# Performance work log

Measured on AMD Instinct MI355X. Metric: run time of the kernel, lower is better.

Reference implementation:

```python
import jax, jax.numpy as jnp
import numpy as np

THRESHOLD = 0.5
NEG_POS_RATIO = 3
ALPHA = 1.0
B, P, C, O = 64, 8732, 81, 32


def setup_inputs() -> dict:
    key = jax.random.key(0)
    k1, k2, k3, k4, k5, k6 = jax.random.split(key, 6)
    pred_locs = jax.random.normal(k1, (B, P, 4), dtype=jnp.float32)
    pred_scores = jax.random.normal(k2, (B, P, C), dtype=jnp.float32)
    # valid ground-truth corner boxes: sample center/size, convert to xy, clip to [0,1]
    ctr = jax.random.uniform(k3, (B, O, 2), minval=0.1, maxval=0.9)
    wh = jax.random.uniform(k4, (B, O, 2), minval=0.05, maxval=0.4)
    boxes = jnp.clip(jnp.concatenate([ctr - wh / 2, ctr + wh / 2], axis=-1), 0.0, 1.0)
    labels = jax.random.randint(k5, (B, O), 1, C, dtype=jnp.int64)
    pc = jax.random.uniform(k6, (P, 2), minval=0.05, maxval=0.95)
    pwh = jax.random.uniform(jax.random.fold_in(k6, 1), (P, 2), minval=0.05, maxval=0.3)
    priors_cxcy = jnp.concatenate([pc, pwh], axis=-1)
    return {"pred_locs": pred_locs, "pred_scores": pred_scores,
            "boxes": boxes, "labels": labels, "priors_cxcy": priors_cxcy}


def _jaccard(b, priors_xy):
    # b: [O,4] xy, priors_xy: [P,4] xy -> [O,P]
    lo = jnp.maximum(b[:, None, :2], priors_xy[None, :, :2])
    hi = jnp.minimum(b[:, None, 2:], priors_xy[None, :, 2:])
    inter = jnp.prod(jnp.clip(hi - lo, 0.0), axis=-1)
    area_b = jnp.prod(b[:, 2:] - b[:, :2], axis=-1)
    area_p = jnp.prod(priors_xy[:, 2:] - priors_xy[:, :2], axis=-1)
    return inter / (area_b[:, None] + area_p[None, :] - inter)


def _forward(pred_locs, pred_scores, boxes, labels, priors_cxcy):
    priors_xy = jnp.concatenate([priors_cxcy[:, :2] - priors_cxcy[:, 2:] / 2,
                                 priors_cxcy[:, :2] + priors_cxcy[:, 2:] / 2], axis=1)
    n_obj = boxes.shape[1]

    def match(b, l):
        ov = _jaccard(b, priors_xy)                      # [O,P]
        ov_fp = jnp.max(ov, axis=0)                      # [P]
        obj_fp = jnp.argmax(ov, axis=0)                  # [P]
        prior_fo = jnp.argmax(ov, axis=1)                # [O]
        obj_fp = obj_fp.at[prior_fo].set(jnp.arange(n_obj))
        ov_fp = ov_fp.at[prior_fo].set(1.0)
        lab = jnp.where(ov_fp < THRESHOLD, 0, l[obj_fp]) # [P]
        pt = b[obj_fp]                                   # [P,4] xy
        c = jnp.concatenate([(pt[:, 2:] + pt[:, :2]) / 2, pt[:, 2:] - pt[:, :2]], axis=1)
        g = jnp.concatenate([(c[:, :2] - priors_cxcy[:, :2]) / (priors_cxcy[:, 2:] / 10),
                             jnp.log(c[:, 2:] / priors_cxcy[:, 2:]) * 5], axis=1)
        return g, lab

    true_locs, true_classes = jax.vmap(match)(boxes, labels)  # [B,P,4], [B,P]

    pos = true_classes != 0                                   # [B,P]
    n_pos = jnp.sum(pos, axis=1)                              # [B]
    n_pos_total = jnp.sum(n_pos).astype(pred_locs.dtype)

    # L1Loss (mean over positive elements, 4 coords each)
    loc_abs = jnp.abs(pred_locs - true_locs) * pos[..., None].astype(pred_locs.dtype)
    loc_loss = jnp.sum(loc_abs) / (n_pos_total * 4.0)

    # per-prior cross entropy
    logp = jax.nn.log_softmax(pred_scores, axis=-1)           # [B,P,C]
    ce = -jnp.take_along_axis(logp, true_classes[..., None], axis=-1)[..., 0]  # [B,P]

    posf = pos.astype(ce.dtype)
    conf_pos_sum = jnp.sum(ce * posf)
    conf_neg = jnp.where(pos, 0.0, ce)
    conf_neg_sorted = -jnp.sort(-conf_neg, axis=1)            # descending
    ranks = jnp.arange(ce.shape[1])[None, :]
    hard = ranks < (NEG_POS_RATIO * n_pos)[:, None]
    conf_hard_neg_sum = jnp.sum(conf_neg_sorted * hard.astype(ce.dtype))

    conf_loss = (conf_hard_neg_sum + conf_pos_sum) / n_pos_total
    return conf_loss + ALPHA * loc_loss


def reference(pred_locs, pred_scores, boxes, labels, priors_cxcy):
    return _forward(pred_locs, pred_scores, boxes, labels, priors_cxcy)
```

## Files before the change

kernel.cpp:

```cpp
#include <hip/hip_runtime.h>

#define BB 64
#define PP 8732
#define OO 32
#define CC 81
#define NEGPOS 3
#define NCH_B 32
#define CHB 273
#define NCEB 137

typedef float f32x4 __attribute__((ext_vector_type(4), aligned(4)));

#define WS_BESTP  0
#define WS_CENEG  (WS_BESTP + BB*NCH_B*OO*8)
#define WS_CEPOS  (WS_CENEG + BB*PP*4)
#define WS_LSUMB  (WS_CEPOS + BB*NCEB*16)
#define WS_NPOSB  (WS_LSUMB + BB*NCEB*16)
#define WS_HARDB  (WS_NPOSB + BB*NCEB*16)
#define WS_DONE   (WS_HARDB + BB*4)

__global__ __launch_bounds__(512) void match_obj(
    const float* __restrict__ boxes, const float* __restrict__ priors,
    unsigned long long* __restrict__ bestp, int* __restrict__ done)
{
    const int b = blockIdx.y, ch = blockIdx.x, tid = threadIdx.x;
    __shared__ float sbx[OO * 4];
    __shared__ unsigned long long sred[8 * OO];
    if (tid < OO * 4) sbx[tid] = boxes[b * OO * 4 + tid];
    if (ch == 0 && b == 0 && tid == 0) *done = 0;
    __syncthreads();

    const int o = tid & 31, sub = tid >> 5;
    const float b0 = sbx[o*4+0], b1 = sbx[o*4+1], b2 = sbx[o*4+2], b3 = sbx[o*4+3];
    const float barea = (b2 - b0) * (b3 - b1);
    const int base = ch * CHB;
    unsigned long long best = 0ull;
    for (int i = sub; i < CHB; i += 16) {
        int p = base + i;
        if (p >= PP) break;
        float4 pr = ((const float4*)priors)[p];
        float plx = pr.x - pr.z * 0.5f, ply = pr.y - pr.w * 0.5f;
        float phx = pr.x + pr.z * 0.5f, phy = pr.y + pr.w * 0.5f;
        float parea = pr.z * pr.w;
        float lox = fmaxf(b0, plx), loy = fmaxf(b1, ply);
        float hix = fminf(b2, phx), hiy = fminf(b3, phy);
        float inter = fmaxf(hix - lox, 0.0f) * fmaxf(hiy - loy, 0.0f);
        float iou = inter / (barea + parea - inter);
        unsigned long long enc =
            ((unsigned long long)__float_as_uint(iou) << 32) | (unsigned)(~(unsigned)p);
        best = (enc > best) ? enc : best;
    }
    unsigned long long w = __shfl_down(best, 32, 64);
    best = (w > best) ? w : best;
    const int wid = tid >> 6, lane = tid & 63;
    if (lane < 32) sred[wid * OO + o] = best;
    __syncthreads();
    if (tid < OO) {
        unsigned long long m = 0ull;
#pragma unroll
        for (int wv = 0; wv < 8; ++wv) {
            unsigned long long v = sred[wv * OO + tid];
            m = (v > m) ? v : m;
        }
        bestp[(b * NCH_B + ch) * OO + tid] = m;
    }
}

__global__ __launch_bounds__(256) void ce_match(
    const float* __restrict__ scores, const float* __restrict__ pred_locs,
    const float* __restrict__ boxes, const int* __restrict__ labels,
    const float* __restrict__ priors,
    const unsigned long long* __restrict__ bestp,
    float* __restrict__ ce_neg, float* __restrict__ cepos4,
    float* __restrict__ lsum4, int* __restrict__ npos4)
{
    const int b = blockIdx.y, ch = blockIdx.x, tid = threadIdx.x;
    const int base = ch * 64;
    __shared__ float sbx[OO * 4];
    __shared__ int   slab[OO];
    __shared__ int   spfo[OO];
    __shared__ unsigned long long sred[4 * OO];

    {
        const unsigned long long* __restrict__ bp_ = bestp + (long long)b * (NCH_B * OO);
        unsigned long long m0 = bp_[tid];
        unsigned long long m1 = bp_[tid + 256];
        unsigned long long m2 = bp_[tid + 512];
        unsigned long long m3 = bp_[tid + 768];
        m0 = (m1 > m0) ? m1 : m0;
        m2 = (m3 > m2) ? m3 : m2;
        m0 = (m2 > m0) ? m2 : m0;
        unsigned long long t2 = __shfl_down(m0, 32, 64);
        m0 = (t2 > m0) ? t2 : m0;
        if ((tid & 63) < 32) sred[(tid >> 6) * OO + (tid & 31)] = m0;
    }
    if (tid < OO * 4) sbx[tid] = boxes[b * OO * 4 + tid];
    if (tid >= 224)   slab[tid - 224] = labels[b * OO + (tid - 224)];
    __syncthreads();
    if (tid < OO) {
        unsigned long long m = sred[tid];
#pragma unroll
        for (int w = 1; w < 4; ++w) {
            unsigned long long v = sred[w * OO + tid];
            m = (v > m) ? v : m;
        }
        spfo[tid] = (int)(~(unsigned)(m & 0xFFFFFFFFull));
    }
    __syncthreads();

    const int g = tid >> 2, j = tid & 3;
    const int p = base + g;
    float posc = 0.0f, lsum = 0.0f; int lpos = 0;

    if (p < PP) {
        const long long bp = (long long)b * PP + p;
        const float* __restrict__ v = scores + bp * CC;

        float d[21];
#pragma unroll
        for (int k = 0; k < 5; ++k) {
            f32x4 t4 = *(const f32x4*)(v + (4 * k + j) * 4);
            d[4*k+0] = t4.x; d[4*k+1] = t4.y; d[4*k+2] = t4.z; d[4*k+3] = t4.w;
        }
        d[20] = (j == 0) ? v[80] : -3.0e38f;

        float4 pr = ((const float4*)priors)[p];
        float plx = pr.x - pr.z * 0.5f, ply = pr.y - pr.w * 0.5f;
        float phx = pr.x + pr.z * 0.5f, phy = pr.y + pr.w * 0.5f;
        float parea = pr.z * pr.w;
        unsigned long long eb = 0ull;
#pragma unroll
        for (int k = 0; k < 8; ++k) {
            const int oo = j * 8 + k;
            float c0 = sbx[oo*4+0], c1 = sbx[oo*4+1], c2 = sbx[oo*4+2], c3 = sbx[oo*4+3];
            float lox = fmaxf(c0, plx), loy = fmaxf(c1, ply);
            float hix = fminf(c2, phx), hiy = fminf(c3, phy);
            float inter = fmaxf(hix - lox, 0.0f) * fmaxf(hiy - loy, 0.0f);
            float iou = inter / ((c2 - c0) * (c3 - c1) + parea - inter);
            unsigned long long enc =
                ((unsigned long long)__float_as_uint(iou) << 32) | (unsigned)(~(unsigned)oo);
            eb = (enc > eb) ? enc : eb;
        }
        {
            unsigned long long t = __shfl_xor(eb, 1, 64); eb = (t > eb) ? t : eb;
            t = __shfl_xor(eb, 2, 64);                    eb = (t > eb) ? t : eb;
        }
        int o = (int)(~(unsigned)(eb & 0xFFFFFFFFull));
        float ov = __uint_as_float((unsigned)(eb >> 32));

#pragma unroll
        for (int oo = 0; oo < OO; ++oo)
            if (spfo[oo] == p) { o = oo; ov = 1.0f; }
        const int l = (ov < 0.5f) ? 0 : slab[o];

        float m = d[20];
#pragma unroll
        for (int i = 0; i < 20; ++i) m = fmaxf(m, d[i]);
        m = fmaxf(m, __shfl_xor(m, 1, 64));
        m = fmaxf(m, __shfl_xor(m, 2, 64));

        float s = 0.0f;
#pragma unroll
        for (int i = 0; i < 21; ++i) s += __expf(d[i] - m);

        float vl = 0.0f;
        if (l == 80) { if (j == 0) vl = d[20]; }
        else { int c = l >> 2; if ((c & 3) == j) vl = d[4 * (c >> 2) + (l & 3)]; }

        s  += __shfl_xor(s, 1, 64);   s  += __shfl_xor(s, 2, 64);
        vl += __shfl_xor(vl, 1, 64);  vl += __shfl_xor(vl, 2, 64);

        float ce = m + __logf(s) - vl;
        if (j == 0) {
            ce_neg[bp] = (l != 0) ? 0.0f : ce;
            if (l != 0) {
                posc = ce; lpos = 1;
                float b0 = sbx[o*4+0], b1 = sbx[o*4+1], b2 = sbx[o*4+2], b3 = sbx[o*4+3];
                float gx = ((b0 + b2) * 0.5f - pr.x) / (pr.z * 0.1f);
                float gy = ((b1 + b3) * 0.5f - pr.y) / (pr.w * 0.1f);
                float gw = logf((b2 - b0) / pr.z) * 5.0f;
                float gh = logf((b3 - b1) / pr.w) * 5.0f;
                float4 pl = ((const float4*)pred_locs)[bp];
                lsum = fabsf(pl.x - gx) + fabsf(pl.y - gy)
                     + fabsf(pl.z - gw) + fabsf(pl.w - gh);
            }
        }
    }

    for (int off = 32; off > 0; off >>= 1) {
        posc += __shfl_down(posc, off, 64);
        lsum += __shfl_down(lsum, off, 64);
        lpos += __shfl_down(lpos, off, 64);
    }
    if ((tid & 63) == 0) {
        const int w = tid >> 6, idx = (b * NCEB + ch) * 4 + w;
        cepos4[idx] = posc;
        lsum4[idx]  = lsum;
        npos4[idx]  = lpos;
    }
}

__device__ __forceinline__ void suffix_select(
    int* hist, int nbins, unsigned rem, unsigned* sel, int* wred, int tid)
{
    const int nb = nbins >> 9;
    const int base = tid * nb;
    int tot = 0;
    for (int i = 0; i < nb; ++i) tot += hist[base + i];
    const int lane = tid & 63, w = tid >> 6;
    int s = tot;
#pragma unroll
    for (int off = 1; off < 64; off <<= 1) {
        int v = __shfl_down(s, off, 64);
        if (lane + off < 64) s += v;
    }
    if (lane == 0) wred[w] = s;
    __syncthreads();
    int after = s - tot;
    for (int ww = w + 1; ww < 8; ++ww) after += wred[ww];
    int cum = after;
    for (int i = nb - 1; i >= 0; --i) {
        int h = hist[base + i];
        if ((unsigned)cum < rem && (unsigned)(cum + h) >= rem) {
            sel[0] = (unsigned)(base + i);
            sel[1] = rem - (unsigned)cum;
        }
        cum += h;
    }
    __syncthreads();
}

__global__ __launch_bounds__(512) void topk_kernel(
    const float* __restrict__ ce_neg, const int* __restrict__ npos4,
    const float* __restrict__ cepos4, const float* __restrict__ lsum4,
    float* __restrict__ hard_b, int* __restrict__ done, float* __restrict__ out)
{
    __shared__ float sv[PP];
    __shared__ int hist[4096];
    __shared__ int wred[8];
    __shared__ unsigned sel[2];
    __shared__ float sr[8];
    __shared__ int sKred[8];
    const int b = blockIdx.x, tid = threadIdx.x;

    for (int i = tid; i < 4096; i += 512) hist[i] = 0;
    {
        int n = 0;
        for (int c = tid; c < NCEB; c += 512) {
            const int4 nn = ((const int4*)npos4)[b * NCEB + c];
            n += ((nn.x + nn.y) + nn.z) + nn.w;
        }
        for (int off = 32; off > 0; off >>= 1) n += __shfl_down(n, off, 64);
        if ((tid & 63) == 0) sKred[tid >> 6] = n;
    }
    __syncthreads();

    for (int p = tid; p < PP; p += 512) {
        float v = ce_neg[b * PP + p];
        sv[p] = v;
        atomicAdd(&hist[__float_as_uint(v) >> 20], 1);
    }
    int K;
    {
        int n = 0;
#pragma unroll
        for (int w = 0; w < 8; ++w) n += sKred[w];
        K = NEGPOS * n;
        if (K > PP) K = PP;
    }
    __syncthreads();

    float hard = 0.0f;
    if (K > 0) {
        suffix_select(hist, 4096, (unsigned)K, sel, wred, tid);
        const unsigned b1 = sel[0], rem1 = sel[1];

        for (int i = tid; i < 1024; i += 512) hist[i] = 0;
        __syncthreads();
        for (int p = tid; p < PP; p += 512) {
            unsigned u = __float_as_uint(sv[p]);
            if ((u >> 20) == b1) atomicAdd(&hist[(u >> 10) & 1023], 1);
        }
        __syncthreads();
        suffix_select(hist, 1024, rem1, sel, wred, tid);
        const unsigned b2 = sel[0], rem2 = sel[1];
        const unsigned pre2 = (b1 << 20) | (b2 << 10);

        for (int i = tid; i < 1024; i += 512) hist[i] = 0;
        __syncthreads();
        for (int p = tid; p < PP; p += 512) {
            unsigned u = __float_as_uint(sv[p]);
            if ((u >> 10) == (pre2 >> 10)) atomicAdd(&hist[u & 1023], 1);
        }
        __syncthreads();
        suffix_select(hist, 1024, rem2, sel, wred, tid);
        const unsigned prefix = pre2 | sel[0];
        const unsigned remaining = sel[1];

        float sgt = 0.0f;
        for (int p = tid; p < PP; p += 512) {
            unsigned u = __float_as_uint(sv[p]);
            if (u > prefix) sgt += sv[p];
        }
        for (int off = 32; off > 0; off >>= 1) sgt += __shfl_down(sgt, off, 64);
        if ((tid & 63) == 0) sr[tid >> 6] = sgt;
        __syncthreads();
        if (tid == 0) {
            hard = 0.0f;
#pragma unroll
            for (int w = 0; w < 8; ++w) hard += sr[w];
            hard += __uint_as_float(prefix) * (float)remaining;
        }
    }
    __shared__ int sticket;
    if (tid == 0) {
        hard_b[b] = hard;
        __threadfence();
        sticket = atomicAdd(done, 1);
    }
    __syncthreads();
    if (sticket != BB - 1) return;

    float cpos = 0.0f, labs = 0.0f, chard = 0.0f; int n = 0;
    for (int i = tid; i < BB * NCEB; i += 512) {
        const float4 c4 = ((const float4*)cepos4)[i];
        const float4 l4 = ((const float4*)lsum4)[i];
        const int4  n4 = ((const int4*)npos4)[i];
        cpos += ((c4.x + c4.y) + c4.z) + c4.w;
        labs += ((l4.x + l4.y) + l4.z) + l4.w;
        n    += ((n4.x + n4.y) + n4.z) + n4.w;
    }
    if (tid < BB) chard = atomicAdd(&hard_b[tid], 0.0f);
    for (int off = 32; off > 0; off >>= 1) {
        cpos  += __shfl_down(cpos, off, 64);
        labs  += __shfl_down(labs, off, 64);
        chard += __shfl_down(chard, off, 64);
        n     += __shfl_down(n, off, 64);
    }
    __shared__ float f0[8], f1[8], f2[8];
    __shared__ int i3[8];
    if ((tid & 63) == 0) { int w = tid >> 6; f0[w] = cpos; f1[w] = labs; f2[w] = chard; i3[w] = n; }
    __syncthreads();
    if (tid == 0) {
        float a = 0.0f, bs = 0.0f, c = 0.0f; int nt = 0;
#pragma unroll
        for (int w = 0; w < 8; ++w) { a += f0[w]; bs += f1[w]; c += f2[w]; nt += i3[w]; }
        float nf = (float)nt;
        out[0] = (c + a) / nf + bs / (nf * 4.0f);
    }
}

extern "C" void kernel_launch(void* const* d_in, const int* in_sizes, int n_in,
                              void* d_out, int out_size, void* d_ws, size_t ws_size,
                              hipStream_t stream) {
    const float* pred_locs   = (const float*)d_in[0];
    const float* pred_scores = (const float*)d_in[1];
    const float* boxes       = (const float*)d_in[2];
    const int*   labels      = (const int*)d_in[3];
    const float* priors      = (const float*)d_in[4];
    float* out = (float*)d_out;

    char* ws = (char*)d_ws;
    unsigned long long* bestp = (unsigned long long*)(ws + WS_BESTP);
    float* ce_neg  = (float*)(ws + WS_CENEG);
    float* cepos4  = (float*)(ws + WS_CEPOS);
    float* lsum4   = (float*)(ws + WS_LSUMB);
    int*   npos4   = (int*)(ws + WS_NPOSB);
    float* hard_b  = (float*)(ws + WS_HARDB);
    int*   done    = (int*)(ws + WS_DONE);

    match_obj<<<dim3(NCH_B, BB), 512, 0, stream>>>(boxes, priors, bestp, done);
    ce_match<<<dim3(NCEB, BB), 256, 0, stream>>>(pred_scores, pred_locs, boxes, labels,
                                                 priors, bestp,
                                                 ce_neg, cepos4, lsum4, npos4);
    topk_kernel<<<BB, 512, 0, stream>>>(ce_neg, npos4, cepos4, lsum4, hard_b, done, out);
}
```

Measured before the change: 304.2 us.

## Process two priors per thread group in ce_match and use per-prior override table

Each ce_match block now covers 128 priors instead of 64, with every 4-lane group handling two priors whose score loads are both issued before any compute. This is meant to raise memory-level parallelism and amortize the per-block bestp reduction over more work. The 32-iteration scan comparing each prior against the forced-match table is replaced by a shared-memory lookup filled with atomicMax. The cost is higher register pressure from holding two 21-float score arrays, and half as many blocks in the grid.

```diff
diff --git a/kernel.cpp b/kernel.cpp
--- a/kernel.cpp
+++ b/kernel.cpp
@@ -8,6 +8,7 @@
 #define NCH_B 32
 #define CHB 273
 #define NCEB 137
+#define NCE2 69
 
 typedef float f32x4 __attribute__((ext_vector_type(4), aligned(4)));
 
@@ -66,6 +67,77 @@
     }
 }
 
+__device__ __forceinline__ void ce_body(
+    const float d[21], const float* __restrict__ priors,
+    const float* sbx, const int* slab, const int* sovr,
+    const float* __restrict__ pred_locs, float* __restrict__ ce_neg,
+    long long bp, int p, int lp, int j,
+    float& posc, float& lsum, int& lpos)
+{
+    float4 pr = ((const float4*)priors)[p];
+    float plx = pr.x - pr.z * 0.5f, ply = pr.y - pr.w * 0.5f;
+    float phx = pr.x + pr.z * 0.5f, phy = pr.y + pr.w * 0.5f;
+    float parea = pr.z * pr.w;
+    unsigned long long eb = 0ull;
+#pragma unroll
+    for (int k = 0; k < 8; ++k) {
+        const int oo = j * 8 + k;
+        float c0 = sbx[oo*4+0], c1 = sbx[oo*4+1], c2 = sbx[oo*4+2], c3 = sbx[oo*4+3];
+        float lox = fmaxf(c0, plx), loy = fmaxf(c1, ply);
+        float hix = fminf(c2, phx), hiy = fminf(c3, phy);
+        float inter = fmaxf(hix - lox, 0.0f) * fmaxf(hiy - loy, 0.0f);
+        float iou = inter / ((c2 - c0) * (c3 - c1) + parea - inter);
+        unsigned long long enc =
+            ((unsigned long long)__float_as_uint(iou) << 32) | (unsigned)(~(unsigned)oo);
+        eb = (enc > eb) ? enc : eb;
+    }
+    {
+        unsigned long long t = __shfl_xor(eb, 1, 64); eb = (t > eb) ? t : eb;
+        t = __shfl_xor(eb, 2, 64);                    eb = (t > eb) ? t : eb;
+    }
+    int o = (int)(~(unsigned)(eb & 0xFFFFFFFFull));
+    float ov = __uint_as_float((unsigned)(eb >> 32));
+
+    {
+        int oa = sovr[lp];
+        if (oa >= 0) { o = oa; ov = 1.0f; }
+    }
+    const int l = (ov < 0.5f) ? 0 : slab[o];
+
+    float m = d[20];
+#pragma unroll
+    for (int i = 0; i < 20; ++i) m = fmaxf(m, d[i]);
+    m = fmaxf(m, __shfl_xor(m, 1, 64));
+    m = fmaxf(m, __shfl_xor(m, 2, 64));
+
+    float s = 0.0f;
+#pragma unroll
+    for (int i = 0; i < 21; ++i) s += __expf(d[i] - m);
+
+    float vl = 0.0f;
+    if (l == 80) { if (j == 0) vl = d[20]; }
+    else { int c = l >> 2; if ((c & 3) == j) vl = d[4 * (c >> 2) + (l & 3)]; }
+
+    s  += __shfl_xor(s, 1, 64);   s  += __shfl_xor(s, 2, 64);
+    vl += __shfl_xor(vl, 1, 64);  vl += __shfl_xor(vl, 2, 64);
+
+    float ce = m + __logf(s) - vl;
+    if (j == 0) {
+        ce_neg[bp] = (l != 0) ? 0.0f : ce;
+        if (l != 0) {
+            posc = ce; lpos = 1;
+            float b0 = sbx[o*4+0], b1 = sbx[o*4+1], b2 = sbx[o*4+2], b3 = sbx[o*4+3];
+            float gx = ((b0 + b2) * 0.5f - pr.x) / (pr.z * 0.1f);
+            float gy = ((b1 + b3) * 0.5f - pr.y) / (pr.w * 0.1f);
+            float gw = logf((b2 - b0) / pr.z) * 5.0f;
+            float gh = logf((b3 - b1) / pr.w) * 5.0f;
+            float4 pl = ((const float4*)pred_locs)[bp];
+            lsum = fabsf(pl.x - gx) + fabsf(pl.y - gy)
+                 + fabsf(pl.z - gw) + fabsf(pl.w - gh);
+        }
+    }
+}
+
 __global__ __launch_bounds__(256) void ce_match(
     const float* __restrict__ scores, const float* __restrict__ pred_locs,
     const float* __restrict__ boxes, const int* __restrict__ labels,
@@ -75,10 +147,10 @@
     float* __restrict__ lsum4, int* __restrict__ npos4)
 {
     const int b = blockIdx.y, ch = blockIdx.x, tid = threadIdx.x;
-    const int base = ch * 64;
+    const int base = ch * 128;
     __shared__ float sbx[OO * 4];
     __shared__ int   slab[OO];
-    __shared__ int   spfo[OO];
+    __shared__ int   sovr[128];
     __shared__ unsigned long long sred[4 * OO];
 
     {
@@ -96,6 +168,7 @@
     }
     if (tid < OO * 4) sbx[tid] = boxes[b * OO * 4 + tid];
     if (tid >= 224)   slab[tid - 224] = labels[b * OO + (tid - 224)];
+    if (tid < 128)    sovr[tid] = -1;
     __syncthreads();
     if (tid < OO) {
         unsigned long long m = sred[tid];
@@ -104,99 +177,64 @@
             unsigned long long v = sred[w * OO + tid];
             m = (v > m) ? v : m;
         }
-        spfo[tid] = (int)(~(unsigned)(m & 0xFFFFFFFFull));
-    }
-    __syncthreads();
-
-    const int g = tid >> 2, j = tid & 3;
-    const int p = base + g;
-    float posc = 0.0f, lsum = 0.0f; int lpos = 0;
-
-    if (p < PP) {
-        const long long bp = (long long)b * PP + p;
-        const float* __restrict__ v = scores + bp * CC;
-
-        float d[21];
+        const int pf = (int)(~(unsigned)(m & 0xFFFFFFFFull));
+        const int local = pf - base;
+        if (local >= 0 && local < 128) atomicMax(&sovr[local], tid);
+    }
+    __syncthreads();
+
+    const int wv = tid >> 6, l = tid & 63;
+    const int g = l >> 2, j = tid & 3;
+    const int lpA = wv * 32 + g, lpB = lpA + 16;
+    const int pA = base + lpA, pB = base + lpB;
+
+    float poscA = 0.0f, lsumA = 0.0f; int lposA = 0;
+    float poscB = 0.0f, lsumB = 0.0f; int lposB = 0;
+    const long long bpA = (long long)b * PP + pA;
+    const long long bpB = (long long)b * PP + pB;
+
+    float dA[21], dB[21];
+    const bool vA = pA < PP, vB = pB < PP;
+    if (vA) {
+        const float* __restrict__ v = scores + bpA * CC;
 #pragma unroll
         for (int k = 0; k < 5; ++k) {
             f32x4 t4 = *(const f32x4*)(v + (4 * k + j) * 4);
-            d[4*k+0] = t4.x; d[4*k+1] = t4.y; d[4*k+2] = t4.z; d[4*k+3] = t4.w;
-        }
-        d[20] = (j == 0) ? v[80] : -3.0e38f;
-
-        float4 pr = ((const float4*)priors)[p];
-        float plx = pr.x - pr.z * 0.5f, ply = pr.y - pr.w * 0.5f;
-        float phx = pr.x + pr.z * 0.5f, phy = pr.y + pr.w * 0.5f;
-        float parea = pr.z * pr.w;
-        unsigned long long eb = 0ull;
-#pragma unroll
-        for (int k = 0; k < 8; ++k) {
-            const int oo = j * 8 + k;
-            float c0 = sbx[oo*4+0], c1 = sbx[oo*4+1], c2 = sbx[oo*4+2], c3 = sbx[oo*4+3];
-            float lox = fmaxf(c0, plx), loy = fmaxf(c1, ply);
-            float hix = fminf(c2, phx), hiy = fminf(c3, phy);
-            float inter = fmaxf(hix - lox, 0.0f) * fmaxf(hiy - loy, 0.0f);
-            float iou = inter / ((c2 - c0) * (c3 - c1) + parea - inter);
-            unsigned long long enc =
-                ((unsigned long long)__float_as_uint(iou) << 32) | (unsigned)(~(unsigned)oo);
-            eb = (enc > eb) ? enc : eb;
-        }
-        {
-            unsigned long long t = __shfl_xor(eb, 1, 64); eb = (t > eb) ? t : eb;
-            t = __shfl_xor(eb, 2, 64);                    eb = (t > eb) ? t : eb;
-        }
-        int o = (int)(~(unsigned)(eb & 0xFFFFFFFFull));
-        float ov = __uint_as_float((unsigned)(eb >> 32));
-
-#pragma unroll
-        for (int oo = 0; oo < OO; ++oo)
-            if (spfo[oo] == p) { o = oo; ov = 1.0f; }
-        const int l = (ov < 0.5f) ? 0 : slab[o];
-
-        float m = d[20];
-#pragma unroll
-        for (int i = 0; i < 20; ++i) m = fmaxf(m, d[i]);
-        m = fmaxf(m, __shfl_xor(m, 1, 64));
-        m = fmaxf(m, __shfl_xor(m, 2, 64));
-
-        float s = 0.0f;
-#pragma unroll
-        for (int i = 0; i < 21; ++i) s += __expf(d[i] - m);
-
-        float vl = 0.0f;
-        if (l == 80) { if (j == 0) vl = d[20]; }
-        else { int c = l >> 2; if ((c & 3) == j) vl = d[4 * (c >> 2) + (l & 3)]; }
-
-        s  += __shfl_xor(s, 1, 64);   s  += __shfl_xor(s, 2, 64);
-        vl += __shfl_xor(vl, 1, 64);  vl += __shfl_xor(vl, 2, 64);
-
-        float ce = m + __logf(s) - vl;
-        if (j == 0) {
-            ce_neg[bp] = (l != 0) ? 0.0f : ce;
-            if (l != 0) {
-                posc = ce; lpos = 1;
-                float b0 = sbx[o*4+0], b1 = sbx[o*4+1], b2 = sbx[o*4+2], b3 = sbx[o*4+3];
-                float gx = ((b0 + b2) * 0.5f - pr.x) / (pr.z * 0.1f);
-                float gy = ((b1 + b3) * 0.5f - pr.y) / (pr.w * 0.1f);
-                float gw = logf((b2 - b0) / pr.z) * 5.0f;
-                float gh = logf((b3 - b1) / pr.w) * 5.0f;
-                float4 pl = ((const float4*)pred_locs)[bp];
-                lsum = fabsf(pl.x - gx) + fabsf(pl.y - gy)
-                     + fabsf(pl.z - gw) + fabsf(pl.w - gh);
-            }
-        }
-    }
-
+            dA[4*k+0] = t4.x; dA[4*k+1] = t4.y; dA[4*k+2] = t4.z; dA[4*k+3] = t4.w;
+        }
+        dA[20] = (j == 0) ? v[80] : -3.0e38f;
+    }
+    if (vB) {
+        const float* __restrict__ v = scores + bpB * CC;
+#pragma unroll
+        for (int k = 0; k < 5; ++k) {
+            f32x4 t4 = *(const f32x4*)(v + (4 * k + j) * 4);
+            dB[4*k+0] = t4.x; dB[4*k+1] = t4.y; dB[4*k+2] = t4.z; dB[4*k+3] = t4.w;
+        }
+        dB[20] = (j == 0) ? v[80] : -3.0e38f;
+    }
+
+    if (vA) ce_body(dA, priors, sbx, slab, sovr, pred_locs, ce_neg,
+                    bpA, pA, lpA, j, poscA, lsumA, lposA);
+    if (vB) ce_body(dB, priors, sbx, slab, sovr, pred_locs, ce_neg,
+                    bpB, pB, lpB, j, poscB, lsumB, lposB);
+
+    const int co = 2 * ch + (wv >> 1);
+    const int wA = (wv & 1) * 2;
     for (int off = 32; off > 0; off >>= 1) {
-        posc += __shfl_down(posc, off, 64);
-        lsum += __shfl_down(lsum, off, 64);
-        lpos += __shfl_down(lpos, off, 64);
-    }
-    if ((tid & 63) == 0) {
-        const int w = tid >> 6, idx = (b * NCEB + ch) * 4 + w;
-        cepos4[idx] = posc;
-        lsum4[idx]  = lsum;
-        npos4[idx]  = lpos;
+        poscA += __shfl_down(poscA, off, 64);
+        lsumA += __shfl_down(lsumA, off, 64);
+        lposA += __shfl_down(lposA, off, 64);
+    }
+    for (int off = 32; off > 0; off >>= 1) {
+        poscB += __shfl_down(poscB, off, 64);
+        lsumB += __shfl_down(lsumB, off, 64);
+        lposB += __shfl_down(lposB, off, 64);
+    }
+    if (l == 0 && co < NCEB) {
+        const int idxA = (b * NCEB + co) * 4 + wA;
+        cepos4[idxA]     = poscA;  lsum4[idxA]     = lsumA;  npos4[idxA]     = lposA;
+        cepos4[idxA + 1] = poscB;  lsum4[idxA + 1] = lsumB;  npos4[idxA + 1] = lposB;
     }
 }
 
@@ -370,7 +408,7 @@
     int*   done    = (int*)(ws + WS_DONE);
 
     match_obj<<<dim3(NCH_B, BB), 512, 0, stream>>>(boxes, priors, bestp, done);
-    ce_match<<<dim3(NCEB, BB), 256, 0, stream>>>(pred_scores, pred_locs, boxes, labels,
+    ce_match<<<dim3(NCE2, BB), 256, 0, stream>>>(pred_scores, pred_locs, boxes, labels,
                                                  priors, bestp,
                                                  ce_neg, cepos4, lsum4, npos4);
     topk_kernel<<<BB, 512, 0, stream>>>(ce_neg, npos4, cepos4, lsum4, hard_b, done, out);
```

Measured after the change: 304.8 us (median of 2 runs). No clear change (+0.2%).
